# Kernel optimization log

Hardware: AMD Instinct MI355X
Metric: run time of the kernel (lower is better)

The kernel has to match this reference:

```python
import jax, jax.numpy as jnp
import numpy as np

B, N, D = 2, 2048, 1024
H = 16
HD = D // H
SCALE = HD ** -0.5


def setup_inputs() -> dict:
    key = jax.random.key(0)
    k1, k2, kw, kb = jax.random.split(key, 4)
    x1 = jax.random.normal(k1, (B, N, D), dtype=jnp.float32)
    x2 = jax.random.normal(k2, (B, N, D), dtype=jnp.float32)
    # fused qkv linear: torch nn.Linear(dim, 3*dim): W [3D, D], b [3D]
    bound = 1.0 / np.sqrt(D)
    qkv_w = jax.random.uniform(kw, (3 * D, D), minval=-bound, maxval=bound, dtype=jnp.float32)
    qkv_b = jax.random.uniform(kb, (3 * D,), minval=-bound, maxval=bound, dtype=jnp.float32)
    return {"x1": x1, "x2": x2, "qkv_w": qkv_w, "qkv_b": qkv_b}


def reference(x1, x2, qkv_w, qkv_b):
    # qkv projections (only q from x1 and k,v from x2 are used by the module)
    q1 = (jnp.einsum('bnd,ed->bne', x1, qkv_w[:D]) + qkv_b[:D])
    k2 = (jnp.einsum('bnd,ed->bne', x2, qkv_w[D:2 * D]) + qkv_b[D:2 * D])
    v2 = (jnp.einsum('bnd,ed->bne', x2, qkv_w[2 * D:]) + qkv_b[2 * D:])
    # [B, H, N, HD]
    q1 = q1.reshape(B, N, H, HD).transpose(0, 2, 1, 3)
    k2 = k2.reshape(B, N, H, HD).transpose(0, 2, 1, 3)
    v2 = v2.reshape(B, N, H, HD).transpose(0, 2, 1, 3)
    # explicit QK^T -> softmax -> AV (materializes [B,H,N,N] like the original)
    scores = jnp.einsum('bhqd,bhkd->bhqk', q1, k2) * SCALE
    attn = jax.nn.softmax(scores, axis=-1)
    out = jnp.einsum('bhqk,bhkd->bhqd', attn, v2)
    # [B, N, D]; note original module skips out_proj (never applied in forward)
    return out.transpose(0, 2, 1, 3).reshape(B, N, D)
```

## Files before the change

### kernel.cpp

```cpp
#include <hip/hip_runtime.h>
#include <cstdint>
#include <cstddef>

#define B_   2
#define N_   2048
#define D_   1024
#define H_   16
#define HD_  64
#define QSCALE_ 0.18033688011112042f

typedef unsigned short u16;
typedef unsigned int   u32;
typedef __attribute__((ext_vector_type(8))) short short8;
typedef __attribute__((ext_vector_type(4))) float f32x4;
typedef __attribute__((ext_vector_type(4))) float fl4;
typedef __attribute__((ext_vector_type(4))) unsigned short us4;

__device__ __forceinline__ u16 f2bf(float f) {
  u32 u = __builtin_bit_cast(u32, f);
  u += 0x7fffu + ((u >> 16) & 1u);
  return (u16)(u >> 16);
}

__device__ __forceinline__ void gload16(const void* g, void* l) {
  typedef __attribute__((address_space(1))) unsigned int gu32;
  typedef __attribute__((address_space(3))) unsigned int lu32;
  __builtin_amdgcn_global_load_lds((gu32*)g, (lu32*)l, 16, 0, 0);
}

__global__ void convert_kernel(const fl4* __restrict__ x1, const fl4* __restrict__ x2,
                               const fl4* __restrict__ w,
                               us4* __restrict__ o1, us4* __restrict__ o2,
                               us4* __restrict__ ow) {
  const int NX = (B_ * N_ * D_) / 4;
  const int NW = (3 * D_ * D_) / 4;
  int stride = gridDim.x * blockDim.x;
  for (int i = blockIdx.x * blockDim.x + threadIdx.x; i < NX; i += stride) {
    fl4 a = x1[i];
    us4 r; r.x = f2bf(a.x); r.y = f2bf(a.y); r.z = f2bf(a.z); r.w = f2bf(a.w);
    o1[i] = r;
    fl4 b = x2[i];
    us4 s; s.x = f2bf(b.x); s.y = f2bf(b.y); s.z = f2bf(b.z); s.w = f2bf(b.w);
    o2[i] = s;
    if (i < NW) {
      fl4 c = w[i];
      us4 t; t.x = f2bf(c.x); t.y = f2bf(c.y); t.z = f2bf(c.z); t.w = f2bf(c.w);
      ow[i] = t;
    }
  }
}

__global__ __launch_bounds__(256) void qkv_gemm(
    const u16* __restrict__ x1b, const u16* __restrict__ x2b,
    const u16* __restrict__ wb, const float* __restrict__ bias,
    u16* __restrict__ Qb, u16* __restrict__ Kb, u16* __restrict__ Vtb) {
  const int z = blockIdx.z;
  const u16* X = (z == 0) ? x1b : x2b;
  const u16* W = wb + (size_t)z * D_ * D_;
  const float* bz = bias + z * D_;
  const int m0 = blockIdx.y * 128;
  const int e0 = blockIdx.x * 128;
  const int tid = threadIdx.x;
  const int lane = tid & 63;
  const int w = tid >> 6;
  const int wr = w >> 1, wc = w & 1;
  const int col = lane & 15, quad = lane >> 4;

  __shared__ __align__(16) u16 As[128 * 32];
  __shared__ __align__(16) u16 Bs[128 * 32];

  f32x4 acc[4][4] = {};

  int off0 = w * 2048 + lane * 16;
  int row0 = off0 >> 6;
  int ke0  = (off0 & 63) >> 1;
  int off1 = off0 + 1024;
  int row1 = off1 >> 6;
  int ke1  = (off1 & 63) >> 1;

  const u16* gA0 = X + (size_t)(m0 + row0) * D_ + ke0;
  const u16* gA1 = X + (size_t)(m0 + row1) * D_ + ke1;
  const u16* gB0 = W + (size_t)(e0 + row0) * D_ + ke0;
  const u16* gB1 = W + (size_t)(e0 + row1) * D_ + ke1;
  u16* lA0 = &As[w * 1024];
  u16* lA1 = &As[w * 1024 + 512];
  u16* lB0 = &Bs[w * 1024];
  u16* lB1 = &Bs[w * 1024 + 512];

  for (int k0 = 0; k0 < D_; k0 += 32) {
    __syncthreads();
    gload16(gA0 + k0, lA0);
    gload16(gA1 + k0, lA1);
    gload16(gB0 + k0, lB0);
    gload16(gB1 + k0, lB1);
    __syncthreads();

    short8 a[4], b[4];
#pragma unroll
    for (int i = 0; i < 4; ++i)
      a[i] = *(const short8*)&As[(wr * 64 + i * 16 + col) * 32 + quad * 8];
#pragma unroll
    for (int j = 0; j < 4; ++j)
      b[j] = *(const short8*)&Bs[(wc * 64 + j * 16 + col) * 32 + quad * 8];
#pragma unroll
    for (int i = 0; i < 4; ++i)
#pragma unroll
      for (int j = 0; j < 4; ++j)
        acc[i][j] = __builtin_amdgcn_mfma_f32_16x16x32_bf16(a[i], b[j], acc[i][j], 0, 0, 0);
  }

#pragma unroll
  for (int j = 0; j < 4; ++j) {
    int eg = e0 + wc * 64 + j * 16 + col;
    float bj = bz[eg];
    int h = eg >> 6, d = eg & 63;
#pragma unroll
    for (int i = 0; i < 4; ++i) {
#pragma unroll
      for (int r = 0; r < 4; ++r) {
        int m = m0 + wr * 64 + i * 16 + quad * 4 + r;
        int bb = m >> 11, n = m & (N_ - 1);
        float v = acc[i][j][r] + bj;
        if (z == 0) v *= QSCALE_;
        u16 o = f2bf(v);
        if (z == 0)      Qb [(((size_t)bb * H_ + h) * N_ + n) * HD_ + d] = o;
        else if (z == 1) Kb [(((size_t)bb * H_ + h) * N_ + n) * HD_ + d] = o;
        else             Vtb[(((size_t)bb * H_ + h) * HD_ + d) * N_ + n] = o;
      }
    }
  }
}

__global__ __launch_bounds__(256) void attn_kernel(
    const u16* __restrict__ Qb, const u16* __restrict__ Kb,
    const u16* __restrict__ Vtb, float* __restrict__ out) {
  const int bh = blockIdx.y;
  const int bb = bh >> 4, h = bh & 15;
  const int q0 = blockIdx.x * 64;
  const int tid = threadIdx.x;
  const int lane = tid & 63;
  const int w = tid >> 6;
  const int col = lane & 15, quad = lane >> 4;

  const u16* __restrict__ Q  = Qb  + ((size_t)bh << 17);
  const u16* __restrict__ K  = Kb  + ((size_t)bh << 17);
  const u16* __restrict__ Vt = Vtb + ((size_t)bh << 17);

  __shared__ __align__(16) u16 Ks[64 * 72];
  __shared__ __align__(16) u16 Vs[64 * 72];
  __shared__ __align__(16) u16 P[4][16 * 72];
  u16* Pw = P[w];

  const int qrow = q0 + w * 16 + col;
  short8 qa0 = *(const short8*)&Q[qrow * HD_ + quad * 8];
  short8 qa1 = *(const short8*)&Q[qrow * HD_ + 32 + quad * 8];

  const int srow = tid >> 3;
  const int sseg = (tid & 7) * 8;
  const u16* gK0 = &K[srow * HD_ + sseg];
  const u16* gK1 = &K[(srow + 32) * HD_ + sseg];
  const u16* gV0 = &Vt[srow * N_ + sseg];
  const u16* gV1 = &Vt[(srow + 32) * N_ + sseg];
  u16* lK0 = &Ks[srow * 72 + sseg];
  u16* lK1 = &Ks[(srow + 32) * 72 + sseg];
  u16* lV0 = &Vs[srow * 72 + sseg];
  u16* lV1 = &Vs[(srow + 32) * 72 + sseg];

  f32x4 accO[4] = {};
  float lsum[4] = {0.f, 0.f, 0.f, 0.f};

  short8 kA = *(const short8*)(gK0);
  short8 kB = *(const short8*)(gK1);
  short8 vA = *(const short8*)(gV0);
  short8 vB = *(const short8*)(gV1);

  for (int k0 = 0; k0 < N_; k0 += 64) {
    __syncthreads();
    *(short8*)lK0 = kA;
    *(short8*)lK1 = kB;
    *(short8*)lV0 = vA;
    *(short8*)lV1 = vB;
    if (k0 + 64 < N_) {
      kA = *(const short8*)(gK0 + (k0 + 64) * HD_);
      kB = *(const short8*)(gK1 + (k0 + 64) * HD_);
      vA = *(const short8*)(gV0 + (k0 + 64));
      vB = *(const short8*)(gV1 + (k0 + 64));
    }
    __syncthreads();

    f32x4 s[4] = {};
#pragma unroll
    for (int jn = 0; jn < 4; ++jn) {
      short8 kb0 = *(const short8*)&Ks[(jn * 16 + col) * 72 + quad * 8];
      short8 kb1 = *(const short8*)&Ks[(jn * 16 + col) * 72 + 32 + quad * 8];
      s[jn] = __builtin_amdgcn_mfma_f32_16x16x32_bf16(qa0, kb0, s[jn], 0, 0, 0);
      s[jn] = __builtin_amdgcn_mfma_f32_16x16x32_bf16(qa1, kb1, s[jn], 0, 0, 0);
    }

#pragma unroll
    for (int jn = 0; jn < 4; ++jn)
#pragma unroll
      for (int r = 0; r < 4; ++r) {
        float e = exp2f(s[jn][r]);
        lsum[r] += e;
        Pw[(quad * 4 + r) * 72 + jn * 16 + col] =
            (u16)(__builtin_bit_cast(u32, e) >> 16);
      }
    __asm__ volatile("" ::: "memory");
    short8 pa0 = *(const short8*)&Pw[col * 72 + quad * 8];
    short8 pa1 = *(const short8*)&Pw[col * 72 + 32 + quad * 8];
    __asm__ volatile("" ::: "memory");

#pragma unroll
    for (int jd = 0; jd < 4; ++jd) {
      short8 vb0 = *(const short8*)&Vs[(jd * 16 + col) * 72 + quad * 8];
      short8 vb1 = *(const short8*)&Vs[(jd * 16 + col) * 72 + 32 + quad * 8];
      accO[jd] = __builtin_amdgcn_mfma_f32_16x16x32_bf16(pa0, vb0, accO[jd], 0, 0, 0);
      accO[jd] = __builtin_amdgcn_mfma_f32_16x16x32_bf16(pa1, vb1, accO[jd], 0, 0, 0);
    }
  }

#pragma unroll
  for (int r = 0; r < 4; ++r) {
    float v = lsum[r];
    v += __shfl_xor(v, 1);
    v += __shfl_xor(v, 2);
    v += __shfl_xor(v, 4);
    v += __shfl_xor(v, 8);
    lsum[r] = 1.0f / v;
  }

#pragma unroll
  for (int jd = 0; jd < 4; ++jd)
#pragma unroll
    for (int r = 0; r < 4; ++r) {
      int n = q0 + w * 16 + quad * 4 + r;
      int e = h * HD_ + jd * 16 + col;
      out[((size_t)bb * N_ + n) * D_ + e] = accO[jd][r] * lsum[r];
    }
}

extern "C" void kernel_launch(void* const* d_in, const int* in_sizes, int n_in,
                              void* d_out, int out_size, void* d_ws, size_t ws_size,
                              hipStream_t stream) {
  const float* x1 = (const float*)d_in[0];
  const float* x2 = (const float*)d_in[1];
  const float* qw = (const float*)d_in[2];
  const float* qb = (const float*)d_in[3];
  float* out = (float*)d_out;

  u16* ws   = (u16*)d_ws;
  u16* x1b  = ws;
  u16* x2b  = ws + 4194304;
  u16* wb   = ws + 8388608;
  u16* Qbf  = ws + 11534336;
  u16* Kbf  = ws + 15728640;
  u16* Vtb  = ws + 19922944;
  if (ws_size < (size_t)24117248 * 2) return;

  convert_kernel<<<dim3(1024), dim3(256), 0, stream>>>(
      (const fl4*)x1, (const fl4*)x2, (const fl4*)qw,
      (us4*)x1b, (us4*)x2b, (us4*)wb);

  qkv_gemm<<<dim3(8, 32, 3), dim3(256), 0, stream>>>(
      x1b, x2b, wb, qb, Qbf, Kbf, Vtb);

  attn_kernel<<<dim3(32, 32), dim3(256), 0, stream>>>(Qbf, Kbf, Vtb, out);
}
```

Baseline: 205.7 us.

## Pre-swizzle K/V layouts and double-buffer attention tiles via direct global-to-LDS loads

The QKV GEMM epilogue now writes K with an XOR-swizzled column layout and writes V as contiguous 64x64 transposed chunks, also swizzled, using packed 4-element stores. Because of this, the attention kernel can copy K/V tiles straight from global memory into unpadded LDS with global_load_lds. It double-buffers those tiles so only one barrier is needed per iteration and the next tile loads while the current one computes. The swizzled reads are meant to avoid LDS bank conflicts without padding. An occupancy hint of 3 blocks per CU is added. The risk is relying on the barrier to wait for the async LDS loads, plus extra register pressure from the launch bound.

```diff
diff --git a/kernel.cpp b/kernel.cpp
--- a/kernel.cpp
+++ b/kernel.cpp
@@ -53,7 +53,7 @@
 __global__ __launch_bounds__(256) void qkv_gemm(
     const u16* __restrict__ x1b, const u16* __restrict__ x2b,
     const u16* __restrict__ wb, const float* __restrict__ bias,
-    u16* __restrict__ Qb, u16* __restrict__ Kb, u16* __restrict__ Vtb) {
+    u16* __restrict__ Qb, u16* __restrict__ Kb, u16* __restrict__ Vcb) {
   const int z = blockIdx.z;
   const u16* X = (z == 0) ? x1b : x2b;
   const u16* W = wb + (size_t)z * D_ * D_;
@@ -114,26 +114,45 @@
     int eg = e0 + wc * 64 + j * 16 + col;
     float bj = bz[eg];
     int h = eg >> 6, d = eg & 63;
-#pragma unroll
-    for (int i = 0; i < 4; ++i) {
-#pragma unroll
-      for (int r = 0; r < 4; ++r) {
-        int m = m0 + wr * 64 + i * 16 + quad * 4 + r;
-        int bb = m >> 11, n = m & (N_ - 1);
-        float v = acc[i][j][r] + bj;
-        if (z == 0) v *= QSCALE_;
-        u16 o = f2bf(v);
-        if (z == 0)      Qb [(((size_t)bb * H_ + h) * N_ + n) * HD_ + d] = o;
-        else if (z == 1) Kb [(((size_t)bb * H_ + h) * N_ + n) * HD_ + d] = o;
-        else             Vtb[(((size_t)bb * H_ + h) * HD_ + d) * N_ + n] = o;
+    int dc = d >> 3, dt = d & 7;
+    if (z == 2) {
+#pragma unroll
+      for (int i = 0; i < 4; ++i) {
+        int m  = m0 + wr * 64 + i * 16 + quad * 4;
+        int bb = m >> 11;
+        int nc = (m & (N_ - 1)) >> 6;
+        int no = i * 16 + quad * 4;
+        int p  = (no >> 3) ^ (d & 7);
+        us4 pk;
+#pragma unroll
+        for (int r = 0; r < 4; ++r) pk[r] = f2bf(acc[i][j][r] + bj);
+        *(us4*)&Vcb[((((size_t)bb * H_ + h) * (N_ / 64) + nc) * HD_ + d) * 64
+                    + p * 8 + (no & 7)] = pk;
       }
-    }
-  }
-}
-
-__global__ __launch_bounds__(256) void attn_kernel(
+    } else {
+#pragma unroll
+      for (int i = 0; i < 4; ++i) {
+#pragma unroll
+        for (int r = 0; r < 4; ++r) {
+          int m = m0 + wr * 64 + i * 16 + quad * 4 + r;
+          int bb = m >> 11, n = m & (N_ - 1);
+          float v = acc[i][j][r] + bj;
+          if (z == 0) {
+            v *= QSCALE_;
+            Qb[(((size_t)bb * H_ + h) * N_ + n) * HD_ + d] = f2bf(v);
+          } else {
+            int p = dc ^ (n & 7);
+            Kb[(((size_t)bb * H_ + h) * N_ + n) * HD_ + p * 8 + dt] = f2bf(v);
+          }
+        }
+      }
+    }
+  }
+}
+
+__global__ __launch_bounds__(256, 3) void attn_kernel(
     const u16* __restrict__ Qb, const u16* __restrict__ Kb,
-    const u16* __restrict__ Vtb, float* __restrict__ out) {
+    const u16* __restrict__ Vcb, float* __restrict__ out) {
   const int bh = blockIdx.y;
   const int bb = bh >> 4, h = bh & 15;
   const int q0 = blockIdx.x * 64;
@@ -143,11 +162,11 @@
   const int col = lane & 15, quad = lane >> 4;
 
   const u16* __restrict__ Q  = Qb  + ((size_t)bh << 17);
-  const u16* __restrict__ K  = Kb  + ((size_t)bh << 17);
-  const u16* __restrict__ Vt = Vtb + ((size_t)bh << 17);
-
-  __shared__ __align__(16) u16 Ks[64 * 72];
-  __shared__ __align__(16) u16 Vs[64 * 72];
+  const u16* __restrict__ Kg = Kb  + ((size_t)bh << 17);
+  const u16* __restrict__ Vg = Vcb + ((size_t)bh << 17);
+
+  __shared__ __align__(16) u16 Ks[2][64 * 64];
+  __shared__ __align__(16) u16 Vs[2][64 * 64];
   __shared__ __align__(16) u16 P[4][16 * 72];
   u16* Pw = P[w];
 
@@ -155,44 +174,41 @@
   short8 qa0 = *(const short8*)&Q[qrow * HD_ + quad * 8];
   short8 qa1 = *(const short8*)&Q[qrow * HD_ + 32 + quad * 8];
 
-  const int srow = tid >> 3;
-  const int sseg = (tid & 7) * 8;
-  const u16* gK0 = &K[srow * HD_ + sseg];
-  const u16* gK1 = &K[(srow + 32) * HD_ + sseg];
-  const u16* gV0 = &Vt[srow * N_ + sseg];
-  const u16* gV1 = &Vt[(srow + 32) * N_ + sseg];
-  u16* lK0 = &Ks[srow * 72 + sseg];
-  u16* lK1 = &Ks[(srow + 32) * 72 + sseg];
-  u16* lV0 = &Vs[srow * 72 + sseg];
-  u16* lV1 = &Vs[(srow + 32) * 72 + sseg];
+  const int soff = (tid >> 3) * 64 + (tid & 7) * 8;
 
   f32x4 accO[4] = {};
   float lsum[4] = {0.f, 0.f, 0.f, 0.f};
-
-  short8 kA = *(const short8*)(gK0);
-  short8 kB = *(const short8*)(gK1);
-  short8 vA = *(const short8*)(gV0);
-  short8 vB = *(const short8*)(gV1);
-
-  for (int k0 = 0; k0 < N_; k0 += 64) {
+  const int swz = col & 7;
+
+  {
+    const u16* gk = Kg + soff;
+    const u16* gv = Vg + soff;
+    gload16(gk,        &Ks[0][soff]);
+    gload16(gk + 2048, &Ks[0][soff + 2048]);
+    gload16(gv,        &Vs[0][soff]);
+    gload16(gv + 2048, &Vs[0][soff + 2048]);
+  }
+
+  for (int it = 0; it < N_ / 64; ++it) {
+    const int buf = it & 1;
     __syncthreads();
-    *(short8*)lK0 = kA;
-    *(short8*)lK1 = kB;
-    *(short8*)lV0 = vA;
-    *(short8*)lV1 = vB;
-    if (k0 + 64 < N_) {
-      kA = *(const short8*)(gK0 + (k0 + 64) * HD_);
-      kB = *(const short8*)(gK1 + (k0 + 64) * HD_);
-      vA = *(const short8*)(gV0 + (k0 + 64));
-      vB = *(const short8*)(gV1 + (k0 + 64));
-    }
-    __syncthreads();
-
+    if (it + 1 < N_ / 64) {
+      const int k0 = (it + 1) * 64;
+      const u16* gk = Kg + k0 * 64 + soff;
+      const u16* gv = Vg + k0 * 64 + soff;
+      gload16(gk,        &Ks[buf ^ 1][soff]);
+      gload16(gk + 2048, &Ks[buf ^ 1][soff + 2048]);
+      gload16(gv,        &Vs[buf ^ 1][soff]);
+      gload16(gv + 2048, &Vs[buf ^ 1][soff + 2048]);
+    }
+
+    const u16* Kt = Ks[buf];
     f32x4 s[4] = {};
 #pragma unroll
     for (int jn = 0; jn < 4; ++jn) {
-      short8 kb0 = *(const short8*)&Ks[(jn * 16 + col) * 72 + quad * 8];
-      short8 kb1 = *(const short8*)&Ks[(jn * 16 + col) * 72 + 32 + quad * 8];
+      int base = (jn * 16 + col) * 64 + ((quad ^ swz) * 8);
+      short8 kb0 = *(const short8*)&Kt[base];
+      short8 kb1 = *(const short8*)&Kt[base ^ 32];
       s[jn] = __builtin_amdgcn_mfma_f32_16x16x32_bf16(qa0, kb0, s[jn], 0, 0, 0);
       s[jn] = __builtin_amdgcn_mfma_f32_16x16x32_bf16(qa1, kb1, s[jn], 0, 0, 0);
     }
@@ -211,10 +227,12 @@
     short8 pa1 = *(const short8*)&Pw[col * 72 + 32 + quad * 8];
     __asm__ volatile("" ::: "memory");
 
+    const u16* Vt = Vs[buf];
 #pragma unroll
     for (int jd = 0; jd < 4; ++jd) {
-      short8 vb0 = *(const short8*)&Vs[(jd * 16 + col) * 72 + quad * 8];
-      short8 vb1 = *(const short8*)&Vs[(jd * 16 + col) * 72 + 32 + quad * 8];
+      int base = (jd * 16 + col) * 64 + ((quad ^ swz) * 8);
+      short8 vb0 = *(const short8*)&Vt[base];
+      short8 vb1 = *(const short8*)&Vt[base ^ 32];
       accO[jd] = __builtin_amdgcn_mfma_f32_16x16x32_bf16(pa0, vb0, accO[jd], 0, 0, 0);
       accO[jd] = __builtin_amdgcn_mfma_f32_16x16x32_bf16(pa1, vb1, accO[jd], 0, 0, 0);
     }
@@ -255,7 +273,7 @@
   u16* wb   = ws + 8388608;
   u16* Qbf  = ws + 11534336;
   u16* Kbf  = ws + 15728640;
-  u16* Vtb  = ws + 19922944;
+  u16* Vcb  = ws + 19922944;
   if (ws_size < (size_t)24117248 * 2) return;
 
   convert_kernel<<<dim3(1024), dim3(256), 0, stream>>>(
@@ -263,7 +281,7 @@
       (us4*)x1b, (us4*)x2b, (us4*)wb);
 
   qkv_gemm<<<dim3(8, 32, 3), dim3(256), 0, stream>>>(
-      x1b, x2b, wb, qb, Qbf, Kbf, Vtb);
-
-  attn_kernel<<<dim3(32, 32), dim3(256), 0, stream>>>(Qbf, Kbf, Vtb, out);
-}
+      x1b, x2b, wb, qb, Qbf, Kbf, Vcb);
+
+  attn_kernel<<<dim3(32, 32), dim3(256), 0, stream>>>(Qbf, Kbf, Vcb, out);
+}
```

New measurement: 215.1 us. 1.05x slower.
